# Performance work log

Measured on AMD Instinct MI355X. Metric: run time of the kernel, lower is better.

## Reference

```python
import jax, jax.numpy as jnp
import numpy as np

D_MODEL = 1024
NUM_HEADS = 16
D_K = D_MODEL // NUM_HEADS


def setup_inputs() -> dict:
    key = jax.random.key(0)
    ks = jax.random.split(key, 10)
    s = 1.0 / np.sqrt(D_MODEL)  # ~ torch Linear init scale
    inp = {
        "x": jax.random.normal(ks[0], (2, 2048, D_MODEL), dtype=jnp.float32),
        "Wq": jax.random.uniform(ks[1], (D_MODEL, D_MODEL), jnp.float32, -s, s),
        "bq": jax.random.uniform(ks[2], (D_MODEL,), jnp.float32, -s, s),
        "Wk": jax.random.uniform(ks[3], (D_MODEL, D_MODEL), jnp.float32, -s, s),
        "bk": jax.random.uniform(ks[4], (D_MODEL,), jnp.float32, -s, s),
        "Wv": jax.random.uniform(ks[5], (D_MODEL, D_MODEL), jnp.float32, -s, s),
        "bv": jax.random.uniform(ks[6], (D_MODEL,), jnp.float32, -s, s),
        "Wo": jax.random.uniform(ks[7], (D_MODEL, D_MODEL), jnp.float32, -s, s),
        "bo": jax.random.uniform(ks[8], (D_MODEL,), jnp.float32, -s, s),
        "ln_gamma": jnp.ones((D_MODEL,), jnp.float32),
        "ln_beta": jnp.zeros((D_MODEL,), jnp.float32),
    }
    return inp


def reference(x, Wq, bq, Wk, bk, Wv, bv, Wo, bo, ln_gamma, ln_beta):
    B, S, D = x.shape
    residual = x
    # LayerNorm (eps=1e-5 as torch default)
    mu = jnp.mean(x, axis=-1, keepdims=True)
    var = jnp.mean(jnp.square(x - mu), axis=-1, keepdims=True)
    xn = (x - mu) * jax.lax.rsqrt(var + 1e-5) * ln_gamma + ln_beta
    # QKV projections (torch Linear: y = x @ W^T + b) -> (B, H, S, d_k)
    def proj(W, b):
        return (xn @ W.T + b).reshape(B, S, NUM_HEADS, D_K).transpose(0, 2, 1, 3)
    Q, K, V = proj(Wq, bq), proj(Wk, bk), proj(Wv, bv)
    scores = jnp.einsum("bhqd,bhkd->bhqk", Q, K) / np.sqrt(D_K).astype(np.float32)
    attn = jax.nn.softmax(scores, axis=-1)  # (B, H, S, S); dropout is no-op (eval)
    context = jnp.einsum("bhqk,bhkd->bhqd", attn, V)
    context = context.transpose(0, 2, 1, 3).reshape(B, S, D)
    out = context @ Wo.T + bo
    return out + residual, attn.mean(axis=1)
```

## Files before the change

kernel.cpp:

```cpp
#include <hip/hip_runtime.h>
#include <stdint.h>
#include <stddef.h>

#define DEV static __device__ __forceinline__

typedef float f32x2 __attribute__((ext_vector_type(2)));
typedef float f32x4 __attribute__((ext_vector_type(4)));
typedef float f32x16 __attribute__((ext_vector_type(16)));
typedef unsigned u32x4 __attribute__((ext_vector_type(4)));
typedef __bf16 bf16x8 __attribute__((ext_vector_type(8)));

DEV short f2bf(float f) {
  union { float f; unsigned u; } a; a.f = f;
  unsigned r = a.u + 0x7fffu + ((a.u >> 16) & 1u);
  return (short)(r >> 16);
}

DEV void gld_lds16(const void* g, void* lds) {
  __builtin_amdgcn_global_load_lds(
      (__attribute__((address_space(1))) void*)(void*)g,
      (__attribute__((address_space(3))) void*)lds, 16, 0, 0);
}

DEV f32x4 MFMA(bf16x8 a, bf16x8 b, f32x4 c) {
  return __builtin_amdgcn_mfma_f32_16x16x32_bf16(a, b, c, 0, 0, 0);
}
DEV f32x16 MFMA32(bf16x8 a, bf16x8 b, f32x16 c) {
  return __builtin_amdgcn_mfma_f32_32x32x16_bf16(a, b, c, 0, 0, 0);
}

DEV float ex2(float x) { return __builtin_amdgcn_exp2f(x); }

DEV unsigned cvtpk(float lo, float hi) {
  unsigned r;
  asm("v_cvt_pk_bf16_f32 %0, %1, %2" : "=v"(r) : "v"(lo), "v"(hi));
  return r;
}

DEV float xhalf_max(float v) {
  float a = v, b = v;
  asm volatile("v_permlane32_swap_b32 %0, %1" : "+v"(a), "+v"(b));
  return fmaxf(a, b);
}
DEV float xhalf_sum(float v) {
  float a = v, b = v;
  asm volatile("v_permlane32_swap_b32 %0, %1" : "+v"(a), "+v"(b));
  return a + b;
}

#define LOG2E 1.4426950408889634f


__global__ __launch_bounds__(256) void k_cvtw_ln(
    const float* __restrict__ w0, const float* __restrict__ w1,
    const float* __restrict__ w2, const float* __restrict__ w3,
    short* __restrict__ dst, const float* __restrict__ x,
    const float* __restrict__ g, const float* __restrict__ be,
    short* __restrict__ xn) {
  __shared__ float ps[4], pss[4];
  if (blockIdx.x < 4096) {
    int i = blockIdx.x * 256 + threadIdx.x;
    int sel = i >> 18;
    const float* src = sel == 0 ? w0 : sel == 1 ? w1 : sel == 2 ? w2 : w3;
    int off = (i & 0x3ffff) * 4;
    float4 v = *(const float4*)(src + off);
    short4 o4; o4.x = f2bf(v.x); o4.y = f2bf(v.y); o4.z = f2bf(v.z); o4.w = f2bf(v.w);
    *(short4*)(dst + (size_t)i * 4) = o4;
  } else {
    int row = blockIdx.x - 4096;
    int t = threadIdx.x;
    const float4* xr = (const float4*)(x + (size_t)row * 1024);
    float4 v = xr[t];
    float s = v.x + v.y + v.z + v.w;
    float ss = v.x * v.x + v.y * v.y + v.z * v.z + v.w * v.w;
#pragma unroll
    for (int o = 32; o; o >>= 1) { s += __shfl_down(s, o); ss += __shfl_down(ss, o); }
    int w = t >> 6, lane = t & 63;
    if (lane == 0) { ps[w] = s; pss[w] = ss; }
    __syncthreads();
    float st = ps[0] + ps[1] + ps[2] + ps[3];
    float sst = pss[0] + pss[1] + pss[2] + pss[3];
    float mean = st * (1.0f / 1024.0f);
    float var = sst * (1.0f / 1024.0f) - mean * mean;
    float rstd = rsqrtf(var + 1e-5f);
    float4 gv = ((const float4*)g)[t];
    float4 bv = ((const float4*)be)[t];
    short4 o4;
    o4.x = f2bf((v.x - mean) * rstd * gv.x + bv.x);
    o4.y = f2bf((v.y - mean) * rstd * gv.y + bv.y);
    o4.z = f2bf((v.z - mean) * rstd * gv.z + bv.z);
    o4.w = f2bf((v.w - mean) * rstd * gv.w + bv.w);
    ((short4*)(xn + (size_t)row * 1024))[t] = o4;
  }
}

__global__ __launch_bounds__(256) void k_gemm_qkv(
    const short* __restrict__ xn, const short* __restrict__ wbf,
    const float* __restrict__ bq, const float* __restrict__ bk,
    const float* __restrict__ bv, short* __restrict__ q_ws,
    short* __restrict__ k_ws, short* __restrict__ v_ws) {
  __shared__ __align__(16) short at[128 * 32];
  __shared__ __align__(16) short bt[128 * 32];
  int t = threadIdx.x, lane = t & 63, w = t >> 6;
  int wr = w >> 1, wc = w & 1;
  int z = blockIdx.z;
  int row0 = blockIdx.y * 128, col0 = blockIdx.x * 128;
  const short* A = xn + (size_t)row0 * 1024;
  const short* Bw = wbf + (size_t)z * (1024 * 1024) + (size_t)col0 * 1024;
  f32x4 acc[4][4];
#pragma unroll
  for (int m = 0; m < 4; m++)
#pragma unroll
    for (int n = 0; n < 4; n++) acc[m][n] = (f32x4)0.0f;

  for (int k0 = 0; k0 < 1024; k0 += 32) {
#pragma unroll
    for (int i = 0; i < 2; i++) {
      int c = t + i * 256;
      int r = c >> 2, cc = (c & 3) * 8;
      gld_lds16(A + (size_t)r * 1024 + k0 + cc, &at[c * 8]);
      gld_lds16(Bw + (size_t)r * 1024 + k0 + cc, &bt[c * 8]);
    }
    __syncthreads();
    bf16x8 af[4], bfr[4];
#pragma unroll
    for (int m = 0; m < 4; m++)
      af[m] = *(const bf16x8*)&at[(wr * 64 + m * 16 + (lane & 15)) * 32 + (lane >> 4) * 8];
#pragma unroll
    for (int n = 0; n < 4; n++)
      bfr[n] = *(const bf16x8*)&bt[(wc * 64 + n * 16 + (lane & 15)) * 32 + (lane >> 4) * 8];
#pragma unroll
    for (int m = 0; m < 4; m++)
#pragma unroll
      for (int n = 0; n < 4; n++) acc[m][n] = MFMA(af[m], bfr[n], acc[m][n]);
    __syncthreads();
  }
  const float* bias = z == 0 ? bq : z == 1 ? bk : bv;
  short* dst = z == 0 ? q_ws : z == 1 ? k_ws : v_ws;
  float scal = z == 0 ? (0.125f * LOG2E) : 1.0f;
#pragma unroll
  for (int m = 0; m < 4; m++)
#pragma unroll
    for (int n = 0; n < 4; n++)
#pragma unroll
      for (int r = 0; r < 4; r++) {
        int grow = row0 + wr * 64 + m * 16 + (lane >> 4) * 4 + r;
        int gcol = col0 + wc * 64 + n * 16 + (lane & 15);
        float val = (acc[m][n][r] + bias[gcol]) * scal;
        int bb = grow >> 11, s = grow & 2047, h = gcol >> 6, d = gcol & 63;
        dst[(((size_t)bb * 16 + h) * 2048 + s) * 64 + d] = f2bf(val);
      }
}

__global__ __launch_bounds__(256) void k_trv(const short* __restrict__ v_ws,
                                             short* __restrict__ vt_ws) {
  __shared__ short tile[64][65];
  int bh = blockIdx.y, s0 = blockIdx.x * 64;
  const short* src = v_ws + ((size_t)bh * 2048 + s0) * 64;
  int t = threadIdx.x;
#pragma unroll
  for (int i = 0; i < 4; i++) {
    int c = t + i * 256;
    int r = c >> 4, d4 = (c & 15) * 4;
    short4 v4 = *(const short4*)&src[r * 64 + d4];
    tile[d4 + 0][r] = v4.x; tile[d4 + 1][r] = v4.y;
    tile[d4 + 2][r] = v4.z; tile[d4 + 3][r] = v4.w;
  }
  __syncthreads();
#pragma unroll
  for (int i = 0; i < 4; i++) {
    int c = t + i * 256;
    int d = c >> 4, r4 = (c & 15) * 4;
    short4 o4;
    o4.x = tile[d][r4 + 0]; o4.y = tile[d][r4 + 1];
    o4.z = tile[d][r4 + 2]; o4.w = tile[d][r4 + 3];
    *(short4*)&vt_ws[((size_t)bh * 64 + d) * 2048 + s0 + r4] = o4;
  }
}

__global__ __launch_bounds__(256, 2) void k_attn1(
    const short* __restrict__ q_ws, const short* __restrict__ k_ws,
    const short* __restrict__ vt_ws, short* __restrict__ o_ws,
    float* __restrict__ m_ws, float* __restrict__ l_ws) {
  __shared__ __align__(16) short k_lds[4][64 * 64];
  __shared__ __align__(16) short vt_lds[4][64 * 64];
  int t = threadIdx.x, lane = t & 63, w = t >> 6;
  int hi = lane >> 5, l31 = lane & 31;
  int qt = blockIdx.x, hd = blockIdx.y, b = blockIdx.z;
  int bh = b * 16 + hd;
  int q0 = qt * 128;
  const short* qb = q_ws + (size_t)bh * (2048 * 64);
  const short* kb = k_ws + (size_t)bh * (2048 * 64);
  const short* vtb = vt_ws + (size_t)bh * (64 * 2048);
  int qg = q0 + w * 32 + l31;

  bf16x8 qf[4];
#pragma unroll
  for (int d4 = 0; d4 < 4; d4++)
    qf[d4] = *(const bf16x8*)&qb[(size_t)qg * 64 + d4 * 16 + hi * 8];
  asm volatile("s_waitcnt vmcnt(0)" ::: "memory");

  const short *kp0, *kp1, *vp0, *vp1;
  {
    int c = t, r = c >> 3, j = (c & 7) ^ (r & 7);
    kp0 = kb + (size_t)r * 64 + j * 8;
    vp0 = vtb + (size_t)r * 2048 + j * 8;
  }
  {
    int c = t + 256, r = c >> 3, j = (c & 7) ^ (r & 7);
    kp1 = kb + (size_t)r * 64 + j * 8;
    vp1 = vtb + (size_t)r * 2048 + j * 8;
  }

  int koff[8], voff[8];
#pragma unroll
  for (int d4 = 0; d4 < 4; d4++) {
    int row0 = l31, row1 = 32 + l31;
    koff[2 * d4]     = row0 * 64 + (((d4 * 2 + hi) ^ (row0 & 7)) * 8);
    koff[2 * d4 + 1] = row1 * 64 + (((d4 * 2 + hi) ^ (row1 & 7)) * 8);
    voff[2 * d4]     = koff[2 * d4];
    voff[2 * d4 + 1] = koff[2 * d4 + 1];
  }

#define STG(tl_, buf)                                            \
  {                                                              \
    gld_lds16(kp0 + (size_t)(tl_) * 4096, &k_lds[buf][t * 8]);   \
    gld_lds16(kp1 + (size_t)(tl_) * 4096, &k_lds[buf][(t + 256) * 8]); \
    gld_lds16(vp0 + (size_t)(tl_) * 64, &vt_lds[buf][t * 8]);    \
    gld_lds16(vp1 + (size_t)(tl_) * 64, &vt_lds[buf][(t + 256) * 8]); \
  }

  STG(0, 0);
  STG(1, 1);

  f32x16 Oacc[2];
#pragma unroll
  for (int i = 0; i < 16; i++) { Oacc[0][i] = 0.0f; Oacc[1][i] = 0.0f; }
  float mrun = -1e30f, lrun = 0.0f;
  bf16x8 pb[4];

  for (int it = 0; it < 32; ++it) {
    int tn = it + 2 <= 31 ? it + 2 : 31;
    STG(tn, (it + 2) & 3);
    asm volatile("s_waitcnt vmcnt(8)" ::: "memory");
    __builtin_amdgcn_s_barrier();

    const short* kl = k_lds[it & 3];
    const short* vl = vt_lds[(it + 3) & 3];

    bf16x8 kfr[8], vfr[8];
#pragma unroll
    for (int i = 0; i < 8; i++) kfr[i] = *(const bf16x8*)&kl[koff[i]];
#pragma unroll
    for (int i = 0; i < 8; i++) vfr[i] = *(const bf16x8*)&vl[voff[i]];

    __builtin_amdgcn_s_setprio(1);
    f32x16 S0 = (f32x16)0.0f, S1 = (f32x16)0.0f;
#pragma unroll
    for (int d4 = 0; d4 < 4; d4++) {
      S0 = MFMA32(kfr[2 * d4], qf[d4], S0);
      S1 = MFMA32(kfr[2 * d4 + 1], qf[d4], S1);
    }
    if (it) {
#pragma unroll
      for (int ks = 0; ks < 4; ks++) {
        Oacc[0] = MFMA32(vfr[2 * ks], pb[ks], Oacc[0]);
        Oacc[1] = MFMA32(vfr[2 * ks + 1], pb[ks], Oacc[1]);
      }
    }
    __builtin_amdgcn_s_setprio(0);

    float mt;
    {
      float a[8];
#pragma unroll
      for (int i = 0; i < 8; i++)
        a[i] = fmaxf(fmaxf(S0[i], S0[i + 8]), fmaxf(S1[i], S1[i + 8]));
      float b0 = fmaxf(fmaxf(a[0], a[1]), fmaxf(a[2], a[3]));
      float b1 = fmaxf(fmaxf(a[4], a[5]), fmaxf(a[6], a[7]));
      mt = xhalf_max(fmaxf(b0, b1));
    }
    if (!__all(mt - mrun <= 8.0f)) {
      float mn = fmaxf(mrun, mt);
      float sc_ = ex2(mrun - mn);
      lrun *= sc_;
#pragma unroll
      for (int i = 0; i < 16; i++) { Oacc[0][i] *= sc_; Oacc[1][i] *= sc_; }
      mrun = mn;
    }
    float rs0 = 0.0f, rs1 = 0.0f;
#pragma unroll
    for (int i = 0; i < 16; i++) {
      float p0 = ex2(S0[i] - mrun);
      float p1 = ex2(S1[i] - mrun);
      S0[i] = p0; S1[i] = p1;
      rs0 += p0; rs1 += p1;
    }
    lrun += xhalf_sum(rs0 + rs1);

#pragma unroll
    for (int ks = 0; ks < 4; ks++) {
      unsigned wA, wB, wC, wD;
      if (ks == 0) {
        wA = cvtpk(S0[0], S0[1]);  wB = cvtpk(S0[2], S0[3]);
        wC = cvtpk(S0[4], S0[5]);  wD = cvtpk(S0[6], S0[7]);
      } else if (ks == 1) {
        wA = cvtpk(S0[8], S0[9]);  wB = cvtpk(S0[10], S0[11]);
        wC = cvtpk(S0[12], S0[13]); wD = cvtpk(S0[14], S0[15]);
      } else if (ks == 2) {
        wA = cvtpk(S1[0], S1[1]);  wB = cvtpk(S1[2], S1[3]);
        wC = cvtpk(S1[4], S1[5]);  wD = cvtpk(S1[6], S1[7]);
      } else {
        wA = cvtpk(S1[8], S1[9]);  wB = cvtpk(S1[10], S1[11]);
        wC = cvtpk(S1[12], S1[13]); wD = cvtpk(S1[14], S1[15]);
      }
      asm volatile("v_permlane32_swap_b32 %0, %1" : "+v"(wA), "+v"(wC));
      asm volatile("v_permlane32_swap_b32 %0, %1" : "+v"(wB), "+v"(wD));
      u32x4 uu; uu.x = wA; uu.y = wB; uu.z = wC; uu.w = wD;
      pb[ks] = __builtin_bit_cast(bf16x8, uu);
    }
    __builtin_amdgcn_s_barrier();
  }
  asm volatile("s_waitcnt vmcnt(0)" ::: "memory");
  __builtin_amdgcn_s_barrier();

  {
    const short* vl = vt_lds[3];
    __builtin_amdgcn_s_setprio(1);
#pragma unroll
    for (int ks = 0; ks < 4; ks++) {
      Oacc[0] = MFMA32(*(const bf16x8*)&vl[voff[2 * ks]], pb[ks], Oacc[0]);
      Oacc[1] = MFMA32(*(const bf16x8*)&vl[voff[2 * ks + 1]], pb[ks], Oacc[1]);
    }
    __builtin_amdgcn_s_setprio(0);
  }

  float rl = 1.0f / lrun;
  if (lane < 32) {
    m_ws[bh * 2048 + qg] = mrun;
    l_ws[bh * 2048 + qg] = rl;
  }
#pragma unroll
  for (int dt = 0; dt < 2; dt++)
#pragma unroll
    for (int g = 0; g < 4; g++) {
      short4 o4;
      o4.x = f2bf(Oacc[dt][g * 4 + 0] * rl);
      o4.y = f2bf(Oacc[dt][g * 4 + 1] * rl);
      o4.z = f2bf(Oacc[dt][g * 4 + 2] * rl);
      o4.w = f2bf(Oacc[dt][g * 4 + 3] * rl);
      int d = dt * 32 + g * 8 + hi * 4;
      *(short4*)&o_ws[((size_t)(b * 2048 + qg)) * 1024 + hd * 64 + d] = o4;
    }
}

__global__ __launch_bounds__(256, 3) void k_attn2(
    const short* __restrict__ q_ws, const short* __restrict__ k_ws,
    const float* __restrict__ m_ws, const float* __restrict__ l_ws,
    float* __restrict__ out1) {
  __shared__ __align__(16) short q_lds[2][64 * 64];
  __shared__ __align__(16) short k_lds2[2][128 * 64];
  __shared__ __align__(16) float ml_lds[2][2][64];
  int t = threadIdx.x, lane = t & 63, w = t >> 6;
  int k2 = blockIdx.x * 128, q0 = blockIdx.y * 64, b = blockIdx.z;

  f32x4 pacc[8];
#pragma unroll
  for (int n = 0; n < 8; n++) pacc[n] = (f32x4)0.0f;

#define STAGE2(hh, buf)                                                          \
  {                                                                              \
    int bh_ = b * 16 + (hh);                                                     \
    const short* qb_ = q_ws + (size_t)bh_ * (2048 * 64);                         \
    const short* kb_ = k_ws + (size_t)bh_ * (2048 * 64);                         \
    _Pragma("unroll")                                                            \
    for (int i = 0; i < 2; i++) {                                                \
      int c = t + i * 256;                                                       \
      int r = c >> 3, j = (c & 7) ^ (r & 7);                                     \
      gld_lds16(qb_ + (size_t)(q0 + r) * 64 + j * 8, &q_lds[buf][c * 8]);        \
    }                                                                            \
    _Pragma("unroll")                                                            \
    for (int i = 0; i < 4; i++) {                                                \
      int c = t + i * 256;                                                       \
      int r = c >> 3, j = (c & 7) ^ (r & 7);                                     \
      gld_lds16(kb_ + (size_t)(k2 + r) * 64 + j * 8, &k_lds2[buf][c * 8]);       \
    }                                                                            \
    int cc = w * 8 + (t & 63);                                                   \
    if ((t & 63) < 8) {                                                          \
      const float* src_ = cc < 16 ? &m_ws[(size_t)bh_ * 2048 + q0 + cc * 4]      \
                                  : &l_ws[(size_t)bh_ * 2048 + q0 + (cc - 16) * 4]; \
      gld_lds16(src_, &ml_lds[buf][0][cc * 4]);                                  \
    }                                                                            \
  }

  STAGE2(0, 0);
  int cur = 0;
  for (int h = 0; h < 16; ++h) {
    int hn = h < 15 ? h + 1 : 15;
    STAGE2(hn, cur ^ 1);
    asm volatile("s_waitcnt vmcnt(7)" ::: "memory");
    __builtin_amdgcn_s_barrier();

    const short* ql = q_lds[cur];
    const short* kl = k_lds2[cur];
    bf16x8 qf[2];
#pragma unroll
    for (int kf = 0; kf < 2; kf++) {
      int row = w * 16 + (lane & 15);
      qf[kf] = *(const bf16x8*)&ql[row * 64 + (((kf * 4 + (lane >> 4)) ^ (row & 7)) * 8)];
    }
    f32x4 sc[8];
#pragma unroll
    for (int n = 0; n < 8; n++) sc[n] = (f32x4)0.0f;
#pragma unroll
    for (int kf = 0; kf < 2; kf++)
#pragma unroll
      for (int n = 0; n < 8; n++) {
        int row = n * 16 + (lane & 15);
        bf16x8 kfr = *(const bf16x8*)&kl[row * 64 + (((kf * 4 + (lane >> 4)) ^ (row & 7)) * 8)];
        sc[n] = MFMA(qf[kf], kfr, sc[n]);
      }
    f32x4 mh = *(const f32x4*)&ml_lds[cur][0][w * 16 + (lane >> 4) * 4];
    f32x4 lh = *(const f32x4*)&ml_lds[cur][1][w * 16 + (lane >> 4) * 4];
#pragma unroll
    for (int n = 0; n < 8; n++)
#pragma unroll
      for (int r = 0; r < 4; r++)
        pacc[n][r] += ex2(sc[n][r] - mh[r]) * lh[r];
    __builtin_amdgcn_s_barrier();
    cur ^= 1;
  }

#pragma unroll
  for (int n = 0; n < 8; n++)
#pragma unroll
    for (int r = 0; r < 4; r++) {
      int q = q0 + w * 16 + (lane >> 4) * 4 + r;
      int k = k2 + n * 16 + (lane & 15);
      out1[((size_t)b * 2048 + q) * 2048 + k] = pacc[n][r] * 0.0625f;
    }
}

__global__ __launch_bounds__(256) void k_gemm_out(
    const short* __restrict__ o_ws, const short* __restrict__ wo_bf,
    const float* __restrict__ bo, const float* __restrict__ x,
    float* __restrict__ out0) {
  __shared__ __align__(16) short at[128 * 32];
  __shared__ __align__(16) short bt[128 * 32];
  int t = threadIdx.x, lane = t & 63, w = t >> 6;
  int wr = w >> 1, wc = w & 1;
  int row0 = blockIdx.y * 128, col0 = blockIdx.x * 128;
  const short* A = o_ws + (size_t)row0 * 1024;
  const short* Bw = wo_bf + (size_t)col0 * 1024;
  f32x4 acc[4][4];
#pragma unroll
  for (int m = 0; m < 4; m++)
#pragma unroll
    for (int n = 0; n < 4; n++) acc[m][n] = (f32x4)0.0f;

  for (int k0 = 0; k0 < 1024; k0 += 32) {
#pragma unroll
    for (int i = 0; i < 2; i++) {
      int c = t + i * 256;
      int r = c >> 2, cc = (c & 3) * 8;
      gld_lds16(A + (size_t)r * 1024 + k0 + cc, &at[c * 8]);
      gld_lds16(Bw + (size_t)r * 1024 + k0 + cc, &bt[c * 8]);
    }
    __syncthreads();
    bf16x8 af[4], bfr[4];
#pragma unroll
    for (int m = 0; m < 4; m++)
      af[m] = *(const bf16x8*)&at[(wr * 64 + m * 16 + (lane & 15)) * 32 + (lane >> 4) * 8];
#pragma unroll
    for (int n = 0; n < 4; n++)
      bfr[n] = *(const bf16x8*)&bt[(wc * 64 + n * 16 + (lane & 15)) * 32 + (lane >> 4) * 8];
#pragma unroll
    for (int m = 0; m < 4; m++)
#pragma unroll
      for (int n = 0; n < 4; n++) acc[m][n] = MFMA(af[m], bfr[n], acc[m][n]);
    __syncthreads();
  }
#pragma unroll
  for (int m = 0; m < 4; m++)
#pragma unroll
    for (int n = 0; n < 4; n++)
#pragma unroll
      for (int r = 0; r < 4; r++) {
        int grow = row0 + wr * 64 + m * 16 + (lane >> 4) * 4 + r;
        int gcol = col0 + wc * 64 + n * 16 + (lane & 15);
        float val = acc[m][n][r] + bo[gcol] + x[(size_t)grow * 1024 + gcol];
        out0[(size_t)grow * 1024 + gcol] = val;
      }
}

extern "C" void kernel_launch(void* const* d_in, const int* in_sizes, int n_in,
                              void* d_out, int out_size, void* d_ws, size_t ws_size,
                              hipStream_t stream) {
  (void)in_sizes; (void)n_in; (void)out_size; (void)ws_size;
  const float* x   = (const float*)d_in[0];
  const float* Wq  = (const float*)d_in[1];
  const float* bq  = (const float*)d_in[2];
  const float* Wk  = (const float*)d_in[3];
  const float* bk  = (const float*)d_in[4];
  const float* Wv  = (const float*)d_in[5];
  const float* bv  = (const float*)d_in[6];
  const float* Wo  = (const float*)d_in[7];
  const float* bo  = (const float*)d_in[8];
  const float* lng = (const float*)d_in[9];
  const float* lnb = (const float*)d_in[10];
  float* out0 = (float*)d_out;
  float* out1 = out0 + (size_t)2 * 2048 * 1024;

  char* ws = (char*)d_ws;
  short* xn    = (short*)(ws);
  short* q_ws  = (short*)(ws + 8388608);
  short* k_ws  = (short*)(ws + 16777216);
  short* o_ws  = (short*)(ws + 25165824);
  short* vt_ws = (short*)(ws + 33554432);
  short* wbf   = (short*)(ws + 41943040);
  float* m_ws  = (float*)(ws + 50331648);
  float* l_ws  = (float*)(ws + 50593792);

  k_cvtw_ln<<<8192, 256, 0, stream>>>(Wq, Wk, Wv, Wo, wbf, x, lng, lnb, xn);
  k_gemm_qkv<<<dim3(8, 32, 3), 256, 0, stream>>>(xn, wbf, bq, bk, bv, q_ws, k_ws, o_ws);
  k_trv<<<dim3(32, 32), 256, 0, stream>>>(o_ws, vt_ws);
  k_attn1<<<dim3(16, 16, 2), 256, 0, stream>>>(q_ws, k_ws, vt_ws, o_ws, m_ws, l_ws);
  k_attn2<<<dim3(16, 32, 2), 256, 0, stream>>>(q_ws, k_ws, m_ws, l_ws, out1);
  k_gemm_out<<<dim3(8, 32), 256, 0, stream>>>(o_ws, wbf + (size_t)3 * 1024 * 1024, bo, x, out0);
}
```

Baseline: 166.4 us.

## Stage 128-key tiles in attention loop with double-buffered K and triple-buffered V^T

The flash-attention loop now stages 128-key tiles per iteration instead of 64, halving the number of barriers and loop iterations. K uses two buffers and V^T three, with a wider XOR swizzle for the 128-wide V^T rows. Each iteration processes two 64-key sub-steps while keeping the one-step-delayed PV MFMA. This lowers barrier and issue overhead per key, but the prefetch depth shrinks from two tiles to one, which may expose more global-load latency.

```diff
diff --git a/kernel.cpp b/kernel.cpp
--- a/kernel.cpp
+++ b/kernel.cpp
@@ -182,8 +182,8 @@
     const short* __restrict__ q_ws, const short* __restrict__ k_ws,
     const short* __restrict__ vt_ws, short* __restrict__ o_ws,
     float* __restrict__ m_ws, float* __restrict__ l_ws) {
-  __shared__ __align__(16) short k_lds[4][64 * 64];
-  __shared__ __align__(16) short vt_lds[4][64 * 64];
+  __shared__ __align__(16) short k_lds[2][128 * 64];
+  __shared__ __align__(16) short vt_lds[3][64 * 128];
   int t = threadIdx.x, lane = t & 63, w = t >> 6;
   int hi = lane >> 5, l31 = lane & 31;
   int qt = blockIdx.x, hd = blockIdx.y, b = blockIdx.z;
@@ -200,38 +200,39 @@
     qf[d4] = *(const bf16x8*)&qb[(size_t)qg * 64 + d4 * 16 + hi * 8];
   asm volatile("s_waitcnt vmcnt(0)" ::: "memory");
 
-  const short *kp0, *kp1, *vp0, *vp1;
-  {
-    int c = t, r = c >> 3, j = (c & 7) ^ (r & 7);
-    kp0 = kb + (size_t)r * 64 + j * 8;
-    vp0 = vtb + (size_t)r * 2048 + j * 8;
-  }
-  {
-    int c = t + 256, r = c >> 3, j = (c & 7) ^ (r & 7);
-    kp1 = kb + (size_t)r * 64 + j * 8;
-    vp1 = vtb + (size_t)r * 2048 + j * 8;
+  const short* kp[4];
+  const short* vp[4];
+#pragma unroll
+  for (int i = 0; i < 4; i++) {
+    int c = t + i * 256;
+    int rk = c >> 3, jk = (c & 7) ^ (rk & 7);
+    kp[i] = kb + (size_t)rk * 64 + jk * 8;
+    int rv = c >> 4, lv = (c & 15) ^ (rv & 15);
+    vp[i] = vtb + (size_t)rv * 2048 + lv * 8;
+  }
+
+#define STG(tl_, kbuf_, vbuf_)                                             \
+  {                                                                        \
+    _Pragma("unroll")                                                      \
+    for (int i_ = 0; i_ < 4; i_++)                                         \
+      gld_lds16(kp[i_] + (size_t)(tl_) * 8192,                             \
+                &k_lds[kbuf_][(t + i_ * 256) * 8]);                        \
+    _Pragma("unroll")                                                      \
+    for (int i_ = 0; i_ < 4; i_++)                                         \
+      gld_lds16(vp[i_] + (size_t)(tl_) * 128,                              \
+                &vt_lds[vbuf_][(t + i_ * 256) * 8]);                       \
   }
 
   int koff[8], voff[8];
 #pragma unroll
   for (int d4 = 0; d4 < 4; d4++) {
-    int row0 = l31, row1 = 32 + l31;
-    koff[2 * d4]     = row0 * 64 + (((d4 * 2 + hi) ^ (row0 & 7)) * 8);
-    koff[2 * d4 + 1] = row1 * 64 + (((d4 * 2 + hi) ^ (row1 & 7)) * 8);
-    voff[2 * d4]     = koff[2 * d4];
-    voff[2 * d4 + 1] = koff[2 * d4 + 1];
-  }
-
-#define STG(tl_, buf)                                            \
-  {                                                              \
-    gld_lds16(kp0 + (size_t)(tl_) * 4096, &k_lds[buf][t * 8]);   \
-    gld_lds16(kp1 + (size_t)(tl_) * 4096, &k_lds[buf][(t + 256) * 8]); \
-    gld_lds16(vp0 + (size_t)(tl_) * 64, &vt_lds[buf][t * 8]);    \
-    gld_lds16(vp1 + (size_t)(tl_) * 64, &vt_lds[buf][(t + 256) * 8]); \
-  }
-
-  STG(0, 0);
-  STG(1, 1);
+    koff[2 * d4]     = l31 * 64 + (((d4 * 2 + hi) ^ (l31 & 7)) * 8);
+    koff[2 * d4 + 1] = (32 + l31) * 64 + (((d4 * 2 + hi) ^ ((32 + l31) & 7)) * 8);
+    voff[2 * d4]     = l31 * 128 + (((d4 * 2 + hi) ^ (l31 & 15)) * 8);
+    voff[2 * d4 + 1] = voff[2 * d4] + 32 * 128;
+  }
+
+  STG(0, 0, 0);
 
   f32x16 Oacc[2];
 #pragma unroll
@@ -239,98 +240,102 @@
   float mrun = -1e30f, lrun = 0.0f;
   bf16x8 pb[4];
 
-  for (int it = 0; it < 32; ++it) {
-    int tn = it + 2 <= 31 ? it + 2 : 31;
-    STG(tn, (it + 2) & 3);
+  for (int it = 0; it < 16; ++it) {
+    int tn = it + 1 <= 15 ? it + 1 : 15;
+    STG(tn, (it + 1) & 1, (it + 1) % 3);
     asm volatile("s_waitcnt vmcnt(8)" ::: "memory");
     __builtin_amdgcn_s_barrier();
 
-    const short* kl = k_lds[it & 3];
-    const short* vl = vt_lds[(it + 3) & 3];
-
-    bf16x8 kfr[8], vfr[8];
-#pragma unroll
-    for (int i = 0; i < 8; i++) kfr[i] = *(const bf16x8*)&kl[koff[i]];
-#pragma unroll
-    for (int i = 0; i < 8; i++) vfr[i] = *(const bf16x8*)&vl[voff[i]];
-
+    const short* kl = k_lds[it & 1];
+
+#pragma unroll
+    for (int sub = 0; sub < 2; ++sub) {
+      const short* vprev = sub == 0 ? vt_lds[(it + 2) % 3] : vt_lds[it % 3];
+      const int cx = sub == 0 ? 64 : 0;
+
+      bf16x8 kfr[8], vfr[8];
+#pragma unroll
+      for (int i = 0; i < 8; i++) kfr[i] = *(const bf16x8*)&kl[sub * 4096 + koff[i]];
+#pragma unroll
+      for (int i = 0; i < 8; i++) vfr[i] = *(const bf16x8*)&vprev[voff[i] ^ cx];
+
+      __builtin_amdgcn_s_setprio(1);
+      f32x16 S0 = (f32x16)0.0f, S1 = (f32x16)0.0f;
+#pragma unroll
+      for (int d4 = 0; d4 < 4; d4++) {
+        S0 = MFMA32(kfr[2 * d4], qf[d4], S0);
+        S1 = MFMA32(kfr[2 * d4 + 1], qf[d4], S1);
+      }
+      if (it > 0 || sub > 0) {
+#pragma unroll
+        for (int ks = 0; ks < 4; ks++) {
+          Oacc[0] = MFMA32(vfr[2 * ks], pb[ks], Oacc[0]);
+          Oacc[1] = MFMA32(vfr[2 * ks + 1], pb[ks], Oacc[1]);
+        }
+      }
+      __builtin_amdgcn_s_setprio(0);
+
+      float mt;
+      {
+        float a[8];
+#pragma unroll
+        for (int i = 0; i < 8; i++)
+          a[i] = fmaxf(fmaxf(S0[i], S0[i + 8]), fmaxf(S1[i], S1[i + 8]));
+        float b0 = fmaxf(fmaxf(a[0], a[1]), fmaxf(a[2], a[3]));
+        float b1 = fmaxf(fmaxf(a[4], a[5]), fmaxf(a[6], a[7]));
+        mt = xhalf_max(fmaxf(b0, b1));
+      }
+      if (!__all(mt - mrun <= 8.0f)) {
+        float mn = fmaxf(mrun, mt);
+        float sc_ = ex2(mrun - mn);
+        lrun *= sc_;
+#pragma unroll
+        for (int i = 0; i < 16; i++) { Oacc[0][i] *= sc_; Oacc[1][i] *= sc_; }
+        mrun = mn;
+      }
+      float rs0 = 0.0f, rs1 = 0.0f;
+#pragma unroll
+      for (int i = 0; i < 16; i++) {
+        float p0 = ex2(S0[i] - mrun);
+        float p1 = ex2(S1[i] - mrun);
+        S0[i] = p0; S1[i] = p1;
+        rs0 += p0; rs1 += p1;
+      }
+      lrun += xhalf_sum(rs0 + rs1);
+
+#pragma unroll
+      for (int ks = 0; ks < 4; ks++) {
+        unsigned wA, wB, wC, wD;
+        if (ks == 0) {
+          wA = cvtpk(S0[0], S0[1]);  wB = cvtpk(S0[2], S0[3]);
+          wC = cvtpk(S0[4], S0[5]);  wD = cvtpk(S0[6], S0[7]);
+        } else if (ks == 1) {
+          wA = cvtpk(S0[8], S0[9]);  wB = cvtpk(S0[10], S0[11]);
+          wC = cvtpk(S0[12], S0[13]); wD = cvtpk(S0[14], S0[15]);
+        } else if (ks == 2) {
+          wA = cvtpk(S1[0], S1[1]);  wB = cvtpk(S1[2], S1[3]);
+          wC = cvtpk(S1[4], S1[5]);  wD = cvtpk(S1[6], S1[7]);
+        } else {
+          wA = cvtpk(S1[8], S1[9]);  wB = cvtpk(S1[10], S1[11]);
+          wC = cvtpk(S1[12], S1[13]); wD = cvtpk(S1[14], S1[15]);
+        }
+        asm volatile("v_permlane32_swap_b32 %0, %1" : "+v"(wA), "+v"(wC));
+        asm volatile("v_permlane32_swap_b32 %0, %1" : "+v"(wB), "+v"(wD));
+        u32x4 uu; uu.x = wA; uu.y = wB; uu.z = wC; uu.w = wD;
+        pb[ks] = __builtin_bit_cast(bf16x8, uu);
+      }
+    }
+    __builtin_amdgcn_s_barrier();
+  }
+  asm volatile("s_waitcnt vmcnt(0)" ::: "memory");
+
+  {
+    const short* vl = vt_lds[0];
     __builtin_amdgcn_s_setprio(1);
-    f32x16 S0 = (f32x16)0.0f, S1 = (f32x16)0.0f;
-#pragma unroll
-    for (int d4 = 0; d4 < 4; d4++) {
-      S0 = MFMA32(kfr[2 * d4], qf[d4], S0);
-      S1 = MFMA32(kfr[2 * d4 + 1], qf[d4], S1);
-    }
-    if (it) {
-#pragma unroll
-      for (int ks = 0; ks < 4; ks++) {
-        Oacc[0] = MFMA32(vfr[2 * ks], pb[ks], Oacc[0]);
-        Oacc[1] = MFMA32(vfr[2 * ks + 1], pb[ks], Oacc[1]);
-      }
-    }
-    __builtin_amdgcn_s_setprio(0);
-
-    float mt;
-    {
-      float a[8];
-#pragma unroll
-      for (int i = 0; i < 8; i++)
-        a[i] = fmaxf(fmaxf(S0[i], S0[i + 8]), fmaxf(S1[i], S1[i + 8]));
-      float b0 = fmaxf(fmaxf(a[0], a[1]), fmaxf(a[2], a[3]));
-      float b1 = fmaxf(fmaxf(a[4], a[5]), fmaxf(a[6], a[7]));
-      mt = xhalf_max(fmaxf(b0, b1));
-    }
-    if (!__all(mt - mrun <= 8.0f)) {
-      float mn = fmaxf(mrun, mt);
-      float sc_ = ex2(mrun - mn);
-      lrun *= sc_;
-#pragma unroll
-      for (int i = 0; i < 16; i++) { Oacc[0][i] *= sc_; Oacc[1][i] *= sc_; }
-      mrun = mn;
-    }
-    float rs0 = 0.0f, rs1 = 0.0f;
-#pragma unroll
-    for (int i = 0; i < 16; i++) {
-      float p0 = ex2(S0[i] - mrun);
-      float p1 = ex2(S1[i] - mrun);
-      S0[i] = p0; S1[i] = p1;
-      rs0 += p0; rs1 += p1;
-    }
-    lrun += xhalf_sum(rs0 + rs1);
-
 #pragma unroll
     for (int ks = 0; ks < 4; ks++) {
-      unsigned wA, wB, wC, wD;
-      if (ks == 0) {
-        wA = cvtpk(S0[0], S0[1]);  wB = cvtpk(S0[2], S0[3]);
-        wC = cvtpk(S0[4], S0[5]);  wD = cvtpk(S0[6], S0[7]);
-      } else if (ks == 1) {
-        wA = cvtpk(S0[8], S0[9]);  wB = cvtpk(S0[10], S0[11]);
-        wC = cvtpk(S0[12], S0[13]); wD = cvtpk(S0[14], S0[15]);
-      } else if (ks == 2) {
-        wA = cvtpk(S1[0], S1[1]);  wB = cvtpk(S1[2], S1[3]);
-        wC = cvtpk(S1[4], S1[5]);  wD = cvtpk(S1[6], S1[7]);
-      } else {
-        wA = cvtpk(S1[8], S1[9]);  wB = cvtpk(S1[10], S1[11]);
-        wC = cvtpk(S1[12], S1[13]); wD = cvtpk(S1[14], S1[15]);
-      }
-      asm volatile("v_permlane32_swap_b32 %0, %1" : "+v"(wA), "+v"(wC));
-      asm volatile("v_permlane32_swap_b32 %0, %1" : "+v"(wB), "+v"(wD));
-      u32x4 uu; uu.x = wA; uu.y = wB; uu.z = wC; uu.w = wD;
-      pb[ks] = __builtin_bit_cast(bf16x8, uu);
-    }
-    __builtin_amdgcn_s_barrier();
-  }
-  asm volatile("s_waitcnt vmcnt(0)" ::: "memory");
-  __builtin_amdgcn_s_barrier();
-
-  {
-    const short* vl = vt_lds[3];
-    __builtin_amdgcn_s_setprio(1);
-#pragma unroll
-    for (int ks = 0; ks < 4; ks++) {
-      Oacc[0] = MFMA32(*(const bf16x8*)&vl[voff[2 * ks]], pb[ks], Oacc[0]);
-      Oacc[1] = MFMA32(*(const bf16x8*)&vl[voff[2 * ks + 1]], pb[ks], Oacc[1]);
+      Oacc[0] = MFMA32(*(const bf16x8*)&vl[voff[2 * ks] ^ 64], pb[ks], Oacc[0]);
+      Oacc[1] = MFMA32(*(const bf16x8*)&vl[voff[2 * ks + 1] ^ 64], pb[ks], Oacc[1]);
     }
     __builtin_amdgcn_s_setprio(0);
   }
```

Result: no change. 167.9 us (+0.9%).
